# Kernel optimization log

Measured on AMD Instinct MI355X. Metric: run time of the kernel, lower is better.

The kernel has to match this reference:

```python
import jax, jax.numpy as jnp
import numpy as np

N = 4096
IN_DIM = 256
H = 4        # n_heads
D = 64       # head_dim (out_dim)
NEG_SLOPE = 0.2


def setup_inputs() -> dict:
    key = jax.random.key(0)
    k_h, k_adj, k_zero, k_W, k_a = jax.random.split(key, 5)
    h = jax.random.normal(k_h, (N, IN_DIM), dtype=jnp.float32)
    adj = jax.random.normal(k_adj, (N, N), dtype=jnp.float32)
    keep = jax.random.uniform(k_zero, (N, N)) >= 0.3
    adj_bias = jnp.where(keep, adj, 0.0)
    W = jax.random.normal(k_W, (IN_DIM, H * D), dtype=jnp.float32) * 0.05
    a = jax.random.normal(k_a, (H, 2 * D), dtype=jnp.float32) * 0.05
    return {"h": h, "adj_bias": adj_bias, "W": W, "a": a}


def reference(h, adj_bias, W, a):
    n = h.shape[0]
    Wh = (h @ W).reshape(n, H, D)                       # [N, H, D]
    # (cat([Wh_i, Wh_j]) * a).sum(-1) separates into two rank-1 terms:
    a_i, a_j = a[:, :D], a[:, D:]                       # [H, D] each
    e_i = jnp.einsum('nhd,hd->nh', Wh, a_i)             # score from dest node i
    e_j = jnp.einsum('nhd,hd->nh', Wh, a_j)             # score from src node j
    e = jax.nn.leaky_relu(e_i[:, None, :] + e_j[None, :, :], NEG_SLOPE)  # [N,N,H]
    mask = (adj_bias == 0.0)[:, :, None]                # [N, N, 1]
    e = e + adj_bias[:, :, None]
    e = jnp.where(mask, -jnp.inf, e)
    # rows where every neighbor is masked: force self-loop score 0
    all_masked = jnp.all(mask, axis=1, keepdims=True)   # [N, 1, 1]
    self_loop = jnp.eye(n, dtype=bool)[:, :, None]      # [N, N, 1]
    e = jnp.where(all_masked & self_loop, 0.0, e)
    alpha = jax.nn.softmax(e, axis=1)                   # softmax over sources j
    # dropout: eval mode (p acts as identity), faithful to training=False
    out = jnp.einsum('ijh,jhd->ihd', alpha, Wh).reshape(n, H * D)  # concat heads
    return jax.nn.elu(out)
```

## Files before the change

### kernel.cpp

```cpp
#include <hip/hip_runtime.h>
#include <cstdint>
#include <cstddef>


typedef _Float16 f16x2 __attribute__((ext_vector_type(2)));
typedef _Float16 f16x4 __attribute__((ext_vector_type(4)));
typedef _Float16 f16x8 __attribute__((ext_vector_type(8)));
typedef float f32x4 __attribute__((ext_vector_type(4)));

#define NN 4096

__global__ __launch_bounds__(256) void gemm_wh(
    const float* __restrict__ A, const float* __restrict__ Bw,
    const float* __restrict__ av, float* __restrict__ C,
    _Float16* __restrict__ Vt,
    _Float16* __restrict__ uit, _Float16* __restrict__ ui5t,
    _Float16* __restrict__ ujt, _Float16* __restrict__ uj5t) {
  __shared__ float sA[32][36];
  __shared__ float sB[32][68];
  __shared__ _Float16 sT[64][40];
  const int h  = blockIdx.x;
  const int by = blockIdx.y;
  const int t  = threadIdx.x;
  const int row0 = by * 32, col0 = h * 64;
  const int tc = t & 15, tr = t >> 4;
  float acc[2][4];
  #pragma unroll
  for (int q = 0; q < 2; q++)
    #pragma unroll
    for (int p = 0; p < 4; p++) acc[q][p] = 0.f;

  for (int k0 = 0; k0 < 256; k0 += 32) {
    __syncthreads();
    {
      const int r = t >> 3, k4 = (t & 7) * 4;
      float4 v = *(const float4*)&A[(size_t)(row0 + r) * 256 + k0 + k4];
      sA[k4 + 0][r] = v.x; sA[k4 + 1][r] = v.y;
      sA[k4 + 2][r] = v.z; sA[k4 + 3][r] = v.w;
    }
    #pragma unroll
    for (int q = 0; q < 2; q++) {
      const int u = t + q * 256;
      const int kr = u >> 4, c4 = (u & 15) * 4;
      *(float4*)&sB[kr][c4] =
          *(const float4*)&Bw[(size_t)(k0 + kr) * 256 + col0 + c4];
    }
    __syncthreads();
    #pragma unroll
    for (int kk = 0; kk < 32; kk++) {
      float2 a2 = *(const float2*)&sA[kk][tr * 2];
      float4 bv = *(const float4*)&sB[kk][tc * 4];
      const float bp[4] = {bv.x, bv.y, bv.z, bv.w};
      #pragma unroll
      for (int p = 0; p < 4; p++) {
        acc[0][p] = fmaf(a2.x, bp[p], acc[0][p]);
        acc[1][p] = fmaf(a2.y, bp[p], acc[1][p]);
      }
    }
  }
  #pragma unroll
  for (int q = 0; q < 2; q++) {
    float4 v = make_float4(acc[q][0], acc[q][1], acc[q][2], acc[q][3]);
    *(float4*)&C[(size_t)(row0 + tr * 2 + q) * 256 + col0 + tc * 4] = v;
  }
  {
    float pi[2] = {0.f, 0.f}, pj[2] = {0.f, 0.f};
    #pragma unroll
    for (int q = 0; q < 2; q++)
      #pragma unroll
      for (int p = 0; p < 4; p++) {
        const int d = tc * 4 + p;
        pi[q] = fmaf(acc[q][p], av[h * 128 + d], pi[q]);
        pj[q] = fmaf(acc[q][p], av[h * 128 + 64 + d], pj[q]);
      }
    #pragma unroll
    for (int m = 1; m <= 8; m <<= 1) {
      #pragma unroll
      for (int q = 0; q < 2; q++) {
        pi[q] += __shfl_xor(pi[q], m, 64);
        pj[q] += __shfl_xor(pj[q], m, 64);
      }
    }
    if (tc == 0) {
      #pragma unroll
      for (int q = 0; q < 2; q++) {
        const int row = row0 + tr * 2 + q;
        uit [(size_t)h * NN + row] = (_Float16)__expf(0.2f * pi[q]);
        ui5t[(size_t)h * NN + row] = (_Float16)__expf(pi[q]);
        ujt [(size_t)h * NN + row] = (_Float16)__expf(0.2f * pj[q]);
        uj5t[(size_t)h * NN + row] = (_Float16)__expf(pj[q]);
      }
    }
  }
  #pragma unroll
  for (int q = 0; q < 2; q++)
    #pragma unroll
    for (int p = 0; p < 4; p++)
      sT[tc * 4 + p][tr * 2 + q] = (_Float16)acc[q][p];
  __syncthreads();
  {
    const int dd = t >> 2, j8 = (t & 3) * 8;
    f16x8 w;
    #pragma unroll
    for (int k = 0; k < 8; k++) w[k] = sT[dd][j8 + k];
    *(f16x8*)&Vt[(size_t)(col0 + dd) * NN + row0 + j8] = w;
  }
}

__global__ __launch_bounds__(256, 2) void gat_attn(
    const float* __restrict__ bias, const _Float16* __restrict__ Vt,
    const _Float16* __restrict__ uit, const _Float16* __restrict__ ui5t,
    const _Float16* __restrict__ ujt, const _Float16* __restrict__ uj5t,
    float* __restrict__ P, float* __restrict__ L, int jpc) {
  __shared__ float rawb[64][128];
  __shared__ _Float16 seb[2][64][136];
  const int itile = blockIdx.x;
  const int chunk = blockIdx.y;
  const int tid = threadIdx.x;
  const int lane = tid & 63;
  const int h = __builtin_amdgcn_readfirstlane(tid >> 6);
  const int m = lane & 15;
  const int quad = lane >> 4;
  const int i0 = itile * 64;
  const int j0 = chunk * jpc;
  const int nc = jpc >> 7;

  f32x4 acc[4][5];
  #pragma unroll
  for (int it = 0; it < 4; it++)
    #pragma unroll
    for (int dt = 0; dt < 5; dt++)
      #pragma unroll
      for (int r = 0; r < 4; r++) acc[it][dt][r] = 0.f;

  f16x8 ui8[4], u58[4];
  #pragma unroll
  for (int it = 0; it < 4; it++) {
    const _Float16 u1 = uit [(size_t)h * NN + i0 + it * 16 + m];
    const _Float16 u5 = ui5t[(size_t)h * NN + i0 + it * 16 + m];
    ui8[it] = (f16x8){u1, u1, u1, u1, u1, u1, u1, u1};
    u58[it] = (f16x8){u5, u5, u5, u5, u5, u5, u5, u5};
  }
  const f16x8 kOne = {(_Float16)1.f, (_Float16)1.f, (_Float16)1.f, (_Float16)1.f,
                      (_Float16)1.f, (_Float16)1.f, (_Float16)1.f, (_Float16)1.f};

  const int lr = h * 16 + (lane >> 5);
  const int lc = lane & 31;
  const float* gb = bias + (size_t)(i0 + lr) * NN + j0 + lc * 4;

  auto issue_load = [&](int jc) {
    const float* g = gb + jc * 128;
    #pragma unroll
    for (int q = 0; q < 8; q++) {
      __builtin_amdgcn_global_load_lds(
          (const __attribute__((address_space(1))) uint32_t*)(g + (size_t)(q * 2) * NN),
          (__attribute__((address_space(3))) uint32_t*)&rawb[h * 16 + q * 2][0],
          16, 0, 0);
    }
  };
  auto convert = [&](int buf) {
    #pragma unroll
    for (int rr = 0; rr < 16; rr++) {
      const int r = h * 16 + rr;
      const float2 v = *(const float2*)&rawb[r][lane * 2];
      f16x2 e;
      e[0] = (_Float16)((v.x == 0.f) ? 0.f : __expf(v.x));
      e[1] = (_Float16)((v.y == 0.f) ? 0.f : __expf(v.y));
      *(f16x2*)&seb[buf][r][lane * 2] = e;
    }
  };

  issue_load(0);
  __syncthreads();
  convert(0);

  const _Float16* vb  = Vt + (size_t)(h * 64 + m) * NN + j0 + quad * 8;
  const _Float16* ujb = ujt  + (size_t)h * NN + j0 + quad * 8;
  const _Float16* u5b = uj5t + (size_t)h * NN + j0 + quad * 8;

  for (int jc = 0; jc < nc; jc++) {
    const int buf = jc & 1;
    __syncthreads();
    if (jc + 1 < nc) issue_load(jc + 1);

    const int jb = jc * 128;
    f16x8 bc[4], ec[4], ujc, u5c;
    #pragma unroll
    for (int dt = 0; dt < 4; dt++)
      bc[dt] = *(const f16x8*)(vb + (size_t)(dt * 16) * NN + jb);
    ujc = *(const f16x8*)(ujb + jb);
    u5c = *(const f16x8*)(u5b + jb);
    #pragma unroll
    for (int it = 0; it < 4; it++)
      ec[it] = *(const f16x8*)&seb[buf][it * 16 + m][quad * 8];

    #pragma unroll
    for (int s = 0; s < 4; s++) {
      f16x8 bn[4], en[4], ujn, u5n;
      if (s < 3) {
        const int off = jb + (s + 1) * 32;
        #pragma unroll
        for (int dt = 0; dt < 4; dt++)
          bn[dt] = *(const f16x8*)(vb + (size_t)(dt * 16) * NN + off);
        ujn = *(const f16x8*)(ujb + off);
        u5n = *(const f16x8*)(u5b + off);
        #pragma unroll
        for (int it = 0; it < 4; it++)
          en[it] = *(const f16x8*)&seb[buf][it * 16 + m][(s + 1) * 32 + quad * 8];
      }
      f16x8 a[4];
      #pragma unroll
      for (int it = 0; it < 4; it++)
        a[it] = ec[it] * __builtin_elementwise_max(u58[it] * u5c, ui8[it] * ujc);
      __builtin_amdgcn_s_setprio(1);
      #pragma unroll
      for (int it = 0; it < 4; it++) {
        #pragma unroll
        for (int dt = 0; dt < 4; dt++)
          acc[it][dt] = __builtin_amdgcn_mfma_f32_16x16x32_f16(a[it], bc[dt], acc[it][dt], 0, 0, 0);
        acc[it][4] = __builtin_amdgcn_mfma_f32_16x16x32_f16(a[it], kOne, acc[it][4], 0, 0, 0);
      }
      __builtin_amdgcn_s_setprio(0);
      if (s < 3) {
        #pragma unroll
        for (int dt = 0; dt < 4; dt++) bc[dt] = bn[dt];
        #pragma unroll
        for (int it = 0; it < 4; it++) ec[it] = en[it];
        ujc = ujn; u5c = u5n;
      }
    }

    __syncthreads();
    if (jc + 1 < nc) convert(buf ^ 1);
  }

  const size_t lb = (size_t)(chunk * 4 + h) * NN + i0;
  if (m == 0) {
    #pragma unroll
    for (int it = 0; it < 4; it++)
      #pragma unroll
      for (int r = 0; r < 4; r++)
        L[lb + it * 16 + quad * 4 + r] = acc[it][4][r];
  }
  const size_t pbase = ((size_t)(chunk * 4 + h) * NN + i0) * 64;
  #pragma unroll
  for (int it = 0; it < 4; it++)
    #pragma unroll
    for (int dt = 0; dt < 4; dt++)
      #pragma unroll
      for (int r = 0; r < 4; r++)
        P[pbase + (size_t)(it * 16 + quad * 4 + r) * 64 + dt * 16 + m] = acc[it][dt][r];
}

template <int CHT>
__global__ __launch_bounds__(256) void reduce_out(
    const float* __restrict__ P, const float* __restrict__ L,
    const float* __restrict__ Wh, float* __restrict__ out) {
  const int i0 = blockIdx.x * 16;
  const int h = blockIdx.y;
  const int t = threadIdx.x;
  const int d2 = (t & 31) * 2;
  const int isub = t >> 5;
  #pragma unroll
  for (int ii = 0; ii < 2; ii++) {
    const int i = i0 + isub * 2 + ii;
    float lsum = 0.f;
    float sx = 0.f, sy = 0.f;
    #pragma unroll
    for (int c = 0; c < CHT; c++) {
      lsum += L[(size_t)(c * 4 + h) * NN + i];
      const float2 p = *(const float2*)&P[((size_t)(c * 4 + h) * NN + i) * 64 + d2];
      sx += p.x; sy += p.y;
    }
    const float2 wh = *(const float2*)&Wh[(size_t)i * 256 + h * 64 + d2];
    const bool fb = (lsum == 0.f);
    float ox = fb ? wh.x : sx / lsum;
    float oy = fb ? wh.y : sy / lsum;
    ox = (ox > 0.f) ? ox : (__expf(ox) - 1.f);
    oy = (oy > 0.f) ? oy : (__expf(oy) - 1.f);
    float2 o = make_float2(ox, oy);
    *(float2*)&out[(size_t)i * 256 + h * 64 + d2] = o;
  }
}

extern "C" void kernel_launch(void* const* d_in, const int* in_sizes, int n_in,
                              void* d_out, int out_size, void* d_ws, size_t ws_size,
                              hipStream_t stream) {
  const float* h_in = (const float*)d_in[0];
  const float* adj  = (const float*)d_in[1];
  const float* W    = (const float*)d_in[2];
  const float* a    = (const float*)d_in[3];
  float* out = (float*)d_out;
  float* ws = (float*)d_ws;

  int CH = 8;
  while (CH > 1) {
    size_t floats = 1048576  + 524288  + 32768  +
                    (size_t)CH * (16384 + 1048576);
    if (floats * 4 <= ws_size) break;
    CH >>= 1;
  }
  const int jpc = NN / CH;

  float* Wh = ws;
  _Float16* Vt   = (_Float16*)(ws + 1048576);
  _Float16* uit  = (_Float16*)(ws + 1048576 + 524288);
  _Float16* ui5t = uit + 16384;
  _Float16* ujt  = ui5t + 16384;
  _Float16* uj5t = ujt + 16384;
  float* Lb = ws + 1048576 + 524288 + 32768;
  float* Pb = Lb + (size_t)CH * 16384;

  hipLaunchKernelGGL(gemm_wh, dim3(4, 128), dim3(256), 0, stream,
                     h_in, W, a, Wh, Vt, uit, ui5t, ujt, uj5t);
  hipLaunchKernelGGL(gat_attn, dim3(64, CH), dim3(256), 0, stream,
                     adj, Vt, uit, ui5t, ujt, uj5t, Pb, Lb, jpc);
  switch (CH) {
    case 8: hipLaunchKernelGGL((reduce_out<8>), dim3(256, 4), dim3(256), 0, stream, Pb, Lb, Wh, out); break;
    case 4: hipLaunchKernelGGL((reduce_out<4>), dim3(256, 4), dim3(256), 0, stream, Pb, Lb, Wh, out); break;
    case 2: hipLaunchKernelGGL((reduce_out<2>), dim3(256, 4), dim3(256), 0, stream, Pb, Lb, Wh, out); break;
    default: hipLaunchKernelGGL((reduce_out<1>), dim3(256, 4), dim3(256), 0, stream, Pb, Lb, Wh, out); break;
  }
}
```

Measured before the change: 144.1 us.

## Fuse bias exp conversion into the MFMA loop with swizzled fp32 LDS double buffer

```diff
diff --git a/kernel.cpp b/kernel.cpp
--- a/kernel.cpp
+++ b/kernel.cpp
@@ -112,8 +112,7 @@
     const _Float16* __restrict__ uit, const _Float16* __restrict__ ui5t,
     const _Float16* __restrict__ ujt, const _Float16* __restrict__ uj5t,
     float* __restrict__ P, float* __restrict__ L, int jpc) {
-  __shared__ float rawb[64][128];
-  __shared__ _Float16 seb[2][64][136];
+  __shared__ float seb[2][64][128];
   const int itile = blockIdx.x;
   const int chunk = blockIdx.y;
   const int tid = threadIdx.x;
@@ -144,35 +143,23 @@
   const f16x8 kOne = {(_Float16)1.f, (_Float16)1.f, (_Float16)1.f, (_Float16)1.f,
                       (_Float16)1.f, (_Float16)1.f, (_Float16)1.f, (_Float16)1.f};
 
-  const int lr = h * 16 + (lane >> 5);
-  const int lc = lane & 31;
-  const float* gb = bias + (size_t)(i0 + lr) * NN + j0 + lc * 4;
-
-  auto issue_load = [&](int jc) {
-    const float* g = gb + jc * 128;
+  const int lr2 = lane >> 5;
+  const int lg  = lane & 31;
+  auto issue_load = [&](int jc, int buf) {
     #pragma unroll
     for (int q = 0; q < 8; q++) {
+      const int row = h * 16 + q * 2 + lr2;
+      const int g = lg ^ (row & 7);
+      const float* src = bias + (size_t)(i0 + row) * NN + j0 + jc * 128 + g * 4;
       __builtin_amdgcn_global_load_lds(
-          (const __attribute__((address_space(1))) uint32_t*)(g + (size_t)(q * 2) * NN),
-          (__attribute__((address_space(3))) uint32_t*)&rawb[h * 16 + q * 2][0],
+          (const __attribute__((address_space(1))) uint32_t*)src,
+          (__attribute__((address_space(3))) uint32_t*)&seb[buf][h * 16 + q * 2][0],
           16, 0, 0);
     }
   };
-  auto convert = [&](int buf) {
-    #pragma unroll
-    for (int rr = 0; rr < 16; rr++) {
-      const int r = h * 16 + rr;
-      const float2 v = *(const float2*)&rawb[r][lane * 2];
-      f16x2 e;
-      e[0] = (_Float16)((v.x == 0.f) ? 0.f : __expf(v.x));
-      e[1] = (_Float16)((v.y == 0.f) ? 0.f : __expf(v.y));
-      *(f16x2*)&seb[buf][r][lane * 2] = e;
-    }
-  };
-
-  issue_load(0);
+
+  issue_load(0, 0);
   __syncthreads();
-  convert(0);
 
   const _Float16* vb  = Vt + (size_t)(h * 64 + m) * NN + j0 + quad * 8;
   const _Float16* ujb = ujt  + (size_t)h * NN + j0 + quad * 8;
@@ -180,23 +167,19 @@
 
   for (int jc = 0; jc < nc; jc++) {
     const int buf = jc & 1;
-    __syncthreads();
-    if (jc + 1 < nc) issue_load(jc + 1);
+    if (jc + 1 < nc) issue_load(jc + 1, buf ^ 1);
 
     const int jb = jc * 128;
-    f16x8 bc[4], ec[4], ujc, u5c;
+    f16x8 bc[4], ujc, u5c;
     #pragma unroll
     for (int dt = 0; dt < 4; dt++)
       bc[dt] = *(const f16x8*)(vb + (size_t)(dt * 16) * NN + jb);
     ujc = *(const f16x8*)(ujb + jb);
     u5c = *(const f16x8*)(u5b + jb);
-    #pragma unroll
-    for (int it = 0; it < 4; it++)
-      ec[it] = *(const f16x8*)&seb[buf][it * 16 + m][quad * 8];
 
     #pragma unroll
     for (int s = 0; s < 4; s++) {
-      f16x8 bn[4], en[4], ujn, u5n;
+      f16x8 bn[4], ujn, u5n;
       if (s < 3) {
         const int off = jb + (s + 1) * 32;
         #pragma unroll
@@ -204,14 +187,26 @@
           bn[dt] = *(const f16x8*)(vb + (size_t)(dt * 16) * NN + off);
         ujn = *(const f16x8*)(ujb + off);
         u5n = *(const f16x8*)(u5b + off);
-        #pragma unroll
-        for (int it = 0; it < 4; it++)
-          en[it] = *(const f16x8*)&seb[buf][it * 16 + m][(s + 1) * 32 + quad * 8];
       }
       f16x8 a[4];
       #pragma unroll
-      for (int it = 0; it < 4; it++)
-        a[it] = ec[it] * __builtin_elementwise_max(u58[it] * u5c, ui8[it] * ujc);
+      for (int it = 0; it < 4; it++) {
+        const int R = it * 16 + m;
+        const int g0 = (s * 8 + quad * 2) ^ (R & 7);
+        const int g1 = (s * 8 + quad * 2 + 1) ^ (R & 7);
+        const float4 v0 = *(const float4*)&seb[buf][R][g0 * 4];
+        const float4 v1 = *(const float4*)&seb[buf][R][g1 * 4];
+        f16x8 e;
+        e[0] = (v0.x == 0.f) ? (_Float16)0.f : (_Float16)__expf(v0.x);
+        e[1] = (v0.y == 0.f) ? (_Float16)0.f : (_Float16)__expf(v0.y);
+        e[2] = (v0.z == 0.f) ? (_Float16)0.f : (_Float16)__expf(v0.z);
+        e[3] = (v0.w == 0.f) ? (_Float16)0.f : (_Float16)__expf(v0.w);
+        e[4] = (v1.x == 0.f) ? (_Float16)0.f : (_Float16)__expf(v1.x);
+        e[5] = (v1.y == 0.f) ? (_Float16)0.f : (_Float16)__expf(v1.y);
+        e[6] = (v1.z == 0.f) ? (_Float16)0.f : (_Float16)__expf(v1.z);
+        e[7] = (v1.w == 0.f) ? (_Float16)0.f : (_Float16)__expf(v1.w);
+        a[it] = e * __builtin_elementwise_max(u58[it] * u5c, ui8[it] * ujc);
+      }
       __builtin_amdgcn_s_setprio(1);
       #pragma unroll
       for (int it = 0; it < 4; it++) {
@@ -224,14 +219,11 @@
       if (s < 3) {
         #pragma unroll
         for (int dt = 0; dt < 4; dt++) bc[dt] = bn[dt];
-        #pragma unroll
-        for (int it = 0; it < 4; it++) ec[it] = en[it];
         ujc = ujn; u5c = u5n;
       }
     }
 
     __syncthreads();
-    if (jc + 1 < nc) convert(buf ^ 1);
   }
 
   const size_t lb = (size_t)(chunk * 4 + h) * NN + i0;
```

New measurement: 147.5 us. +2.4%, slower.
